# Kernel tuning notes

Hardware: AMD Instinct MI355X
Metric: run time of the kernel (lower is better)

The kernel has to match this reference:

```python
import jax, jax.numpy as jnp
import numpy as np
import math

B, N, D, H = 2, 2048, 512, 8
DK = D // H
MIN_WL, MAX_WL, BASE, EPS = 3.7, 20.0, 20.0, 0.02


def setup_inputs() -> dict:
    key = jax.random.key(0)
    ks = jax.random.split(key, 8)
    q = jax.random.normal(ks[0], (B, N, D), dtype=jnp.float32)
    k = jax.random.normal(ks[1], (B, N, D), dtype=jnp.float32)
    v = jax.random.normal(ks[2], (B, N, D), dtype=jnp.float32)
    coords = jax.random.normal(ks[3], (B, N, 3), dtype=jnp.float32)
    key_padding_mask = jnp.zeros((B, N), dtype=bool)
    q_proj = jax.random.normal(ks[4], (H, D, DK), dtype=jnp.float32)
    k_proj = jax.random.normal(ks[5], (H, D, DK), dtype=jnp.float32)
    v_proj = jax.random.normal(ks[6], (H, D, DK), dtype=jnp.float32)
    out_w = jax.random.normal(ks[7], (D, D), dtype=jnp.float32) / math.sqrt(D)
    out_b = jnp.zeros((D,), dtype=jnp.float32)
    return {"q": q, "k": k, "v": v, "coords": coords,
            "key_padding_mask": key_padding_mask,
            "q_proj": q_proj, "k_proj": k_proj, "v_proj": v_proj,
            "out_w": out_w, "out_b": out_b}


def reference(q, k, v, coords, key_padding_mask, q_proj, k_proj, v_proj, out_w, out_b):
    b, n, d = q.shape
    h, _, dk = q_proj.shape
    # per-head projections: [b,h,n,dk]
    qh = jnp.einsum('bnd,hdk->bhnk', q, q_proj)
    kh = jnp.einsum('bnd,hdk->bhnk', k, k_proj)
    vh = jnp.einsum('bnd,hdk->bhnk', v, v_proj)
    attn = jnp.einsum('bhik,bhjk->bhij', qh, kh) / math.sqrt(dk)  # [b,h,n,n]
    # pairwise distances [b,1,n,n]
    diff = coords[:, :, None, :] - coords[:, None, :, :]
    dists = jnp.sqrt(jnp.sum(diff * diff, axis=-1))[:, None, :, :]
    # per-head spreads via logspace(0, 1-eps, h, base=BASE)
    logsp = BASE ** jnp.linspace(0.0, 1.0 - EPS, h, dtype=jnp.float32)
    spreads = MIN_WL + (logsp - 1.0) / (BASE - 1.0) * (MAX_WL - MIN_WL)
    spreads = spreads[None, :, None, None]  # [1,h,1,1]
    # clamp small dists up to spread, large dists down to 3*spread (masked anyway)
    d1 = jnp.where(dists < spreads, spreads, dists)            # [b,h,n,n]
    dist_mask = d1 > 3.0 * spreads
    d2 = jnp.where(dist_mask, 3.0 * spreads, d1)
    # RBF scaling, inverted where attn < 0
    rbf = jnp.exp(-(d2 * d2) / (2.0 * spreads * spreads))
    rbf = jnp.where(attn < 0, 1.0 / rbf, rbf)
    attn = attn * rbf
    # padding + distance mask, softmax
    mask = key_padding_mask[:, None, None, :] | dist_mask
    attn = jnp.where(mask, -jnp.inf, attn)
    attn = jax.nn.softmax(attn, axis=-1)
    out = jnp.einsum('bhij,bhjk->bhik', attn, vh)  # [b,h,n,dk]
    out = jnp.transpose(out, (0, 2, 1, 3)).reshape(b, n, d)
    return out @ out_w.T + out_b
```

## Files before the change

### kernel.cpp

```cpp
#include <hip/hip_runtime.h>
#include <hip/hip_bf16.h>
#include <cmath>

typedef __attribute__((ext_vector_type(8))) short bf16x8;
typedef __attribute__((ext_vector_type(4))) float f32x4;
typedef __attribute__((ext_vector_type(4))) short short4v;

#define MFMA16(a,b,c) __builtin_amdgcn_mfma_f32_16x16x32_bf16((a),(b),(c),0,0,0)
#define EXP2F(x) __builtin_amdgcn_exp2f(x)
#define GLOAD_LDS16(g, l) __builtin_amdgcn_global_load_lds( \
    (const __attribute__((address_space(1))) unsigned int*)(g), \
    (__attribute__((address_space(3))) unsigned int*)(l), 16, 0, 0)

__device__ __forceinline__ short f2bf(float x){
  unsigned u = __float_as_uint(x);
  u += 0x7fffu + ((u >> 16) & 1u);
  return (short)(u >> 16);
}
__device__ __forceinline__ float bf2f(short h){
  return __uint_as_float(((unsigned)(unsigned short)h) << 16);
}
__device__ __forceinline__ int swz(int row, int c){ return (row << 3) | (c ^ (row & 7)); }

__global__ void split3(const float* __restrict__ q, const float* __restrict__ k,
                       const float* __restrict__ v,
                       short* __restrict__ q_hi, short* __restrict__ q_lo,
                       short* __restrict__ k_hi, short* __restrict__ k_lo,
                       short* __restrict__ v_hi){
  int y = blockIdx.y;
  int i4 = (blockIdx.x * 256 + threadIdx.x) * 4;
  if(y == 0){
    float4 x = *(const float4*)(q + i4);
    short4v hi, lo;
    float xs[4] = {x.x, x.y, x.z, x.w};
    #pragma unroll
    for(int r=0;r<4;r++){ short h = f2bf(xs[r]); hi[r]=h; lo[r]=f2bf(xs[r]-bf2f(h)); }
    *(short4v*)(q_hi + i4) = hi; *(short4v*)(q_lo + i4) = lo;
  } else if(y == 1){
    float4 x = *(const float4*)(k + i4);
    short4v hi, lo;
    float xs[4] = {x.x, x.y, x.z, x.w};
    #pragma unroll
    for(int r=0;r<4;r++){ short h = f2bf(xs[r]); hi[r]=h; lo[r]=f2bf(xs[r]-bf2f(h)); }
    *(short4v*)(k_hi + i4) = hi; *(short4v*)(k_lo + i4) = lo;
  } else {
    float4 x = *(const float4*)(v + i4);
    short4v hi;
    float xs[4] = {x.x, x.y, x.z, x.w};
    #pragma unroll
    for(int r=0;r<4;r++) hi[r] = f2bf(xs[r]);
    *(short4v*)(v_hi + i4) = hi;
  }
}

__global__ void split_proj4(const float* __restrict__ qp, const float* __restrict__ kp,
                            const float* __restrict__ vp, const float* __restrict__ ow,
                            short* __restrict__ BqHi, short* __restrict__ BqLo,
                            short* __restrict__ BkHi, short* __restrict__ BkLo,
                            short* __restrict__ BvHi,
                            short* __restrict__ WHi,  short* __restrict__ WLo){
  int y = blockIdx.y;
  int i = blockIdx.x * 256 + threadIdx.x;
  int n = i >> 9, d = i & 511;
  int h = n >> 6, c = n & 63;
  long si = (long)((h << 15) | (d << 6) | c);
  if(y == 0){
    float x = qp[si]; short hh = f2bf(x);
    BqHi[i] = hh; BqLo[i] = f2bf(x - bf2f(hh));
  } else if(y == 1){
    float x = kp[si]; short hh = f2bf(x);
    BkHi[i] = hh; BkLo[i] = f2bf(x - bf2f(hh));
  } else if(y == 2){
    BvHi[i] = f2bf(vp[si]);
  } else {
    float x = ow[i]; short hh = f2bf(x);
    WHi[i] = hh; WLo[i] = f2bf(x - bf2f(hh));
  }
}

__global__ __launch_bounds__(256) void gemm_qkv(
    const short* __restrict__ q_hi, const short* __restrict__ q_lo,
    const short* __restrict__ k_hi, const short* __restrict__ k_lo,
    const short* __restrict__ v_hi,
    const short* __restrict__ BqHi, const short* __restrict__ BqLo,
    const short* __restrict__ BkHi, const short* __restrict__ BkLo,
    const short* __restrict__ BvHi,
    short* __restrict__ qhHi, short* __restrict__ qhLo,
    short* __restrict__ khHi, short* __restrict__ khLo,
    short* __restrict__ vt)
{
  constexpr int K = 512;
  __shared__ __attribute__((aligned(16))) short sAhi[128*64];
  __shared__ __attribute__((aligned(16))) short sBhi[64*64];
  __shared__ __attribute__((aligned(16))) short sAlo[128*64];
  __shared__ __attribute__((aligned(16))) short sBlo[64*64];
  const int tid = threadIdx.x;
  const int z = blockIdx.z;
  const bool three = (z < 2);
  const short* Ahi = z==0 ? q_hi : z==1 ? k_hi : v_hi;
  const short* Alo = z==0 ? q_lo : k_lo;
  const short* Bhi = z==0 ? BqHi : z==1 ? BkHi : BvHi;
  const short* Blo = z==0 ? BqLo : BkLo;
  const float scale = z==0 ? 0.125f*1.44269504f : 1.f;
  const int m0 = blockIdx.x * 128, n0 = blockIdx.y * 64;
  const int w = tid >> 6, lane = tid & 63;
  const int wm = (w >> 1) * 64, wn = (w & 1) * 32;
  const int lr = lane & 15, lg = lane >> 4;

  f32x4 acc[4][2];
  for(int i=0;i<4;i++) for(int j=0;j<2;j++) acc[i][j] = f32x4{0.f,0.f,0.f,0.f};

  for(int kt = 0; kt < K; kt += 64){
    __syncthreads();
    for(int u = tid; u < 1024; u += 256){
      int row = u >> 3, c = u & 7;
      long ga = (long)(m0 + row) * K + kt + (c ^ (row & 7))*8;
      GLOAD_LDS16(Ahi + ga, sAhi + u*8);
      if(three) GLOAD_LDS16(Alo + ga, sAlo + u*8);
    }
    for(int u = tid; u < 512; u += 256){
      int row = u >> 3, c = u & 7;
      long ga = (long)(n0 + row) * K + kt + (c ^ (row & 7))*8;
      GLOAD_LDS16(Bhi + ga, sBhi + u*8);
      if(three) GLOAD_LDS16(Blo + ga, sBlo + u*8);
    }
    __syncthreads();
    #pragma unroll
    for(int ks = 0; ks < 2; ks++){
      bf16x8 ah[4], al[4], bh[2], bl[2];
      #pragma unroll
      for(int i=0;i<4;i++){
        int row = wm + i*16 + lr, c = ks*4 + lg;
        ah[i] = *(const bf16x8*)(sAhi + swz(row,c)*8);
        if(three) al[i] = *(const bf16x8*)(sAlo + swz(row,c)*8);
      }
      #pragma unroll
      for(int j=0;j<2;j++){
        int row = wn + j*16 + lr, c = ks*4 + lg;
        bh[j] = *(const bf16x8*)(sBhi + swz(row,c)*8);
        if(three) bl[j] = *(const bf16x8*)(sBlo + swz(row,c)*8);
      }
      #pragma unroll
      for(int i=0;i<4;i++)
        #pragma unroll
        for(int j=0;j<2;j++){
          acc[i][j] = MFMA16(ah[i], bh[j], acc[i][j]);
          if(three){
            acc[i][j] = MFMA16(ah[i], bl[j], acc[i][j]);
            acc[i][j] = MFMA16(al[i], bh[j], acc[i][j]);
          }
        }
    }
  }
  #pragma unroll
  for(int i=0;i<4;i++){
    #pragma unroll
    for(int j=0;j<2;j++){
      int row = m0 + wm + i*16 + lg*4;
      int col = n0 + wn + j*16 + lr;
      if(z == 2){
        int bb = row >> 11;
        int hh = col >> 6, cc = col & 63;
        short4v pk;
        #pragma unroll
        for(int r=0;r<4;r++) pk[r] = f2bf(acc[i][j][r]);
        long idx = ((long)((bb*8 + hh)*64 + cc) << 11) + (row & 2047);
        *(short4v*)(vt + idx) = pk;
      } else {
        short* O0 = z==0 ? qhHi : khHi;
        short* O1 = z==0 ? qhLo : khLo;
        #pragma unroll
        for(int r=0;r<4;r++){
          float v = acc[i][j][r] * scale;
          long idx = (long)(row + r) * 512 + col;
          short hh = f2bf(v);
          O0[idx] = hh;
          O1[idx] = f2bf(v - bf2f(hh));
        }
      }
    }
  }
}

template<int NPROD, int EPI>
__global__ __launch_bounds__(256) void gemm_k(
    const short* __restrict__ Ahi, const short* __restrict__ Alo,
    const short* __restrict__ Bhi, const short* __restrict__ Blo,
    short* __restrict__ O0, short* __restrict__ O1,
    float* __restrict__ Of, const float* __restrict__ bias, float scale)
{
  constexpr int K = 512;
  __shared__ __attribute__((aligned(16))) short sAhi[128*64];
  __shared__ __attribute__((aligned(16))) short sBhi[64*64];
  __shared__ __attribute__((aligned(16))) short sAlo[NPROD==3 ? 128*64 : 8];
  __shared__ __attribute__((aligned(16))) short sBlo[NPROD==3 ? 64*64 : 8];
  const int tid = threadIdx.x;
  const int m0 = blockIdx.x * 128, n0 = blockIdx.y * 64;
  const int w = tid >> 6, lane = tid & 63;
  const int wm = (w >> 1) * 64, wn = (w & 1) * 32;
  const int lr = lane & 15, lg = lane >> 4;

  f32x4 acc[4][2];
  for(int i=0;i<4;i++) for(int j=0;j<2;j++) acc[i][j] = f32x4{0.f,0.f,0.f,0.f};

  for(int kt = 0; kt < K; kt += 64){
    __syncthreads();
    for(int u = tid; u < 1024; u += 256){
      int row = u >> 3, c = u & 7;
      long ga = (long)(m0 + row) * K + kt + (c ^ (row & 7))*8;
      GLOAD_LDS16(Ahi + ga, sAhi + u*8);
      if(NPROD == 3) GLOAD_LDS16(Alo + ga, sAlo + u*8);
    }
    for(int u = tid; u < 512; u += 256){
      int row = u >> 3, c = u & 7;
      long ga = (long)(n0 + row) * K + kt + (c ^ (row & 7))*8;
      GLOAD_LDS16(Bhi + ga, sBhi + u*8);
      if(NPROD == 3) GLOAD_LDS16(Blo + ga, sBlo + u*8);
    }
    __syncthreads();
    #pragma unroll
    for(int ks = 0; ks < 2; ks++){
      bf16x8 ah[4], al[4], bh[2], bl[2];
      #pragma unroll
      for(int i=0;i<4;i++){
        int row = wm + i*16 + lr, c = ks*4 + lg;
        ah[i] = *(const bf16x8*)(sAhi + swz(row,c)*8);
        if(NPROD==3) al[i] = *(const bf16x8*)(sAlo + swz(row,c)*8);
      }
      #pragma unroll
      for(int j=0;j<2;j++){
        int row = wn + j*16 + lr, c = ks*4 + lg;
        bh[j] = *(const bf16x8*)(sBhi + swz(row,c)*8);
        if(NPROD==3) bl[j] = *(const bf16x8*)(sBlo + swz(row,c)*8);
      }
      #pragma unroll
      for(int i=0;i<4;i++)
        #pragma unroll
        for(int j=0;j<2;j++){
          acc[i][j] = MFMA16(ah[i], bh[j], acc[i][j]);
          if(NPROD==3){
            acc[i][j] = MFMA16(ah[i], bl[j], acc[i][j]);
            acc[i][j] = MFMA16(al[i], bh[j], acc[i][j]);
          }
        }
    }
  }
  #pragma unroll
  for(int i=0;i<4;i++){
    #pragma unroll
    for(int j=0;j<2;j++){
      int row = m0 + wm + i*16 + lg*4;
      int col = n0 + wn + j*16 + lr;
      if(EPI == 1){
        int bb = row >> 11;
        int hh = col >> 6, cc = col & 63;
        short4v pk;
        #pragma unroll
        for(int r=0;r<4;r++) pk[r] = f2bf(acc[i][j][r] * scale);
        long idx = ((long)((bb*8 + hh)*64 + cc) << 11) + (row & 2047);
        *(short4v*)(O0 + idx) = pk;
      } else {
        #pragma unroll
        for(int r=0;r<4;r++){
          float v = acc[i][j][r] * scale;
          long idx = (long)(row + r) * 512 + col;
          if(EPI == 0){
            short hh = f2bf(v);
            O0[idx] = hh;
            O1[idx] = f2bf(v - bf2f(hh));
          } else {
            Of[idx] = v + bias[col];
          }
        }
      }
    }
  }
}

struct SpreadArgs { float sig2[8]; float nine[8]; float inv2l[8]; };

__global__ __launch_bounds__(256) void attn_k(
    const short* __restrict__ qhHi, const short* __restrict__ qhLo,
    const short* __restrict__ khHi, const short* __restrict__ khLo,
    const short* __restrict__ vt,
    const float* __restrict__ coords,
    const unsigned char* __restrict__ kpm,
    short* __restrict__ Xhi, short* __restrict__ Xlo,
    SpreadArgs sa)
{
  __shared__ __attribute__((aligned(16))) short sKhi[64*64];
  __shared__ __attribute__((aligned(16))) short sKlo[64*64];
  __shared__ __attribute__((aligned(16))) short sV[64*64];
  __shared__ __attribute__((aligned(16))) short sCjPk[64*8];
  __shared__ float sNj[64];
  __shared__ __attribute__((aligned(16))) short sP[4][16][72];

  const int tid = threadIdx.x, w = tid >> 6, lane = tid & 63;
  const int lr = lane & 15, lg = lane >> 4;
  const int L = blockIdx.x;
  const int xcd = L & 7, ix = L >> 3;
  const int pair = xcd*2 + (ix >> 5);
  const int b = pair >> 3, h = pair & 7, i0 = (ix & 31) * 64;
  const float sig2 = sa.sig2[h], nine = sa.nine[h], inv2l = sa.inv2l[h];
  bf16x8 ones8;
  #pragma unroll
  for(int i=0;i<8;i++) ones8[i] = (short)0x3F80;

  long qrow = (long)(b*2048 + i0 + w*16 + lr) * 512 + h*64;
  bf16x8 qhi[2], qlo[2];
  #pragma unroll
  for(int ks=0; ks<2; ks++){
    qhi[ks] = *(const bf16x8*)(qhHi + qrow + ks*32 + lg*8);
    qlo[ks] = *(const bf16x8*)(qhLo + qrow + ks*32 + lg*8);
  }
  bf16x8 ciA;
  #pragma unroll
  for(int i=0;i<8;i++) ciA[i] = 0;
  {
    long cb = (long)(b*2048 + i0 + w*16 + lr)*3;
    #pragma unroll
    for(int e=0;e<3;e++){
      float c = coords[cb + e];
      short chi = f2bf(c);
      short clo = f2bf(c - bf2f(chi));
      ciA[e] = f2bf(-2.f * bf2f(lg < 2 ? chi : clo));
    }
  }
  float ni[4];
  {
    int r0 = b*2048 + i0 + w*16 + lg*4;
    #pragma unroll
    for(int r=0;r<4;r++){
      float cx = coords[(long)(r0+r)*3 + 0];
      float cy = coords[(long)(r0+r)*3 + 1];
      float cz = coords[(long)(r0+r)*3 + 2];
      ni[r] = cx*cx + cy*cy + cz*cz;
    }
  }
  f32x4 oacc[4];
  for(int c=0;c<4;c++) oacc[c] = f32x4{0.f,0.f,0.f,0.f};
  float m[4], l[4];
  for(int r=0;r<4;r++){ m[r] = -1e30f; l[r] = 0.f; }

  for(int jt=0; jt<32; jt++){
    int j0 = jt*64;
    for(int u=tid; u<512; u+=256){
      int row = u>>3, cc = u&7;
      int cs = cc ^ (row & 7);
      long gk = (long)(b*2048 + j0 + row)*512 + h*64 + cs*8;
      GLOAD_LDS16(khHi + gk, sKhi + u*8);
      GLOAD_LDS16(khLo + gk, sKlo + u*8);
      long gv = ((long)((b*8+h)*64 + row) << 11) + j0 + cs*8;
      GLOAD_LDS16(vt + gv, sV + u*8);
    }
    if(tid < 64){
      long cb = (long)(b*2048 + j0 + tid)*3;
      float cx = coords[cb], cy = coords[cb+1], cz = coords[cb+2];
      short hx = f2bf(cx), hy = f2bf(cy), hz = f2bf(cz);
      bf16x8 pk;
      pk[0] = hx; pk[1] = hy; pk[2] = hz; pk[3] = 0;
      pk[4] = f2bf(cx - bf2f(hx));
      pk[5] = f2bf(cy - bf2f(hy));
      pk[6] = f2bf(cz - bf2f(hz));
      pk[7] = 0;
      *(bf16x8*)(sCjPk + tid*8) = pk;
      sNj[tid] = cx*cx + cy*cy + cz*cz + (kpm[b*2048 + j0 + tid] ? 1e37f : 0.f);
    }
    __syncthreads();

    f32x4 s[4];
    #pragma unroll
    for(int jf=0;jf<4;jf++){
      f32x4 t = f32x4{0.f,0.f,0.f,0.f};
      #pragma unroll
      for(int ks=0;ks<2;ks++){
        int row = jf*16 + lr, c = ks*4 + lg;
        bf16x8 bh = *(const bf16x8*)(sKhi + swz(row,c)*8);
        bf16x8 bl = *(const bf16x8*)(sKlo + swz(row,c)*8);
        t = MFMA16(qhi[ks], bh, t);
        t = MFMA16(qhi[ks], bl, t);
        t = MFMA16(qlo[ks], bh, t);
      }
      s[jf] = t;
    }
    f32x4 d2t[4];
    #pragma unroll
    for(int jf=0;jf<4;jf++){
      bf16x8 cjB;
      #pragma unroll
      for(int i=0;i<8;i++) cjB[i] = 0;
      {
        short4v c4 = *(const short4v*)(sCjPk + (jf*16 + lr)*8 + (lg & 1)*4);
        cjB[0] = c4[0]; cjB[1] = c4[1]; cjB[2] = c4[2];
      }
      float njv = sNj[jf*16 + lr];
      f32x4 cin;
      #pragma unroll
      for(int r=0;r<4;r++) cin[r] = ni[r] + njv;
      d2t[jf] = MFMA16(ciA, cjB, cin);
    }
    #pragma unroll
    for(int jf=0;jf<4;jf++){
      #pragma unroll
      for(int r=0;r<4;r++){
        float d2 = d2t[jf][r];
        float tt = fminf(fmaxf(d2, sig2), nine);
        float arg2 = tt * inv2l;
        float sv = s[jf][r];
        sv *= EXP2F(sv < 0.f ? arg2 : -arg2);
        if(d2 > nine) sv = -1e30f;
        s[jf][r] = sv;
      }
    }
    float pm[4];
    #pragma unroll
    for(int r=0;r<4;r++)
      pm[r] = fmaxf(fmaxf(s[0][r], s[1][r]), fmaxf(s[2][r], s[3][r]));
    #pragma unroll
    for(int d=1; d<16; d<<=1){
      #pragma unroll
      for(int r=0;r<4;r++) pm[r] = fmaxf(pm[r], __shfl_xor(pm[r], d));
    }
    float fr[4];
    #pragma unroll
    for(int r=0;r<4;r++){
      float mn = fmaxf(m[r], pm[r]);
      fr[r] = EXP2F(m[r] - mn);
      m[r] = mn;
      l[r] *= fr[r];
    }
    #pragma unroll
    for(int jf=0;jf<4;jf++)
      #pragma unroll
      for(int r=0;r<4;r++)
        s[jf][r] = EXP2F(s[jf][r] - m[r]);
    #pragma unroll
    for(int c=0;c<4;c++)
      #pragma unroll
      for(int r=0;r<4;r++) oacc[c][r] *= fr[r];
    #pragma unroll
    for(int jf=0;jf<4;jf++)
      #pragma unroll
      for(int r=0;r<4;r++)
        sP[w][lg*4 + r][jf*16 + lr] = f2bf(s[jf][r]);
    f32x4 psacc = f32x4{0.f,0.f,0.f,0.f};
    #pragma unroll
    for(int js=0;js<2;js++){
      union { bf16x8 v8; short4v h4[2]; } pa;
      pa.h4[0] = *(const short4v*)(&sP[w][lr][js*32 + lg*8]);
      pa.h4[1] = *(const short4v*)(&sP[w][lr][js*32 + lg*8 + 4]);
      #pragma unroll
      for(int cf=0; cf<4; cf++){
        int vrow = cf*16 + lr, vc = js*4 + lg;
        bf16x8 vb = *(const bf16x8*)(sV + swz(vrow,vc)*8);
        oacc[cf] = MFMA16(pa.v8, vb, oacc[cf]);
      }
      psacc = MFMA16(pa.v8, ones8, psacc);
    }
    #pragma unroll
    for(int r=0;r<4;r++) l[r] += psacc[r];
    __syncthreads();
  }
  #pragma unroll
  for(int cf=0; cf<4; cf++){
    #pragma unroll
    for(int r=0;r<4;r++){
      float v = oacc[cf][r] / l[r];
      long idx = (long)(b*2048 + i0 + w*16 + lg*4 + r)*512 + h*64 + cf*16 + lr;
      short hh = f2bf(v);
      Xhi[idx] = hh;
      Xlo[idx] = f2bf(v - bf2f(hh));
    }
  }
}

extern "C" void kernel_launch(void* const* d_in, const int* in_sizes, int n_in,
                              void* d_out, int out_size, void* d_ws, size_t ws_size,
                              hipStream_t stream){
  const float* q  = (const float*)d_in[0];
  const float* k  = (const float*)d_in[1];
  const float* v  = (const float*)d_in[2];
  const float* coords = (const float*)d_in[3];
  const unsigned char* kpm = (const unsigned char*)d_in[4];
  const float* qp = (const float*)d_in[5];
  const float* kp = (const float*)d_in[6];
  const float* vp = (const float*)d_in[7];
  const float* ow = (const float*)d_in[8];
  const float* ob = (const float*)d_in[9];
  float* out = (float*)d_out;

  char* ws = (char*)d_ws;
  const size_t S = (size_t)4096*512*2;
  const size_t P = (size_t)512*512*2;
  if(ws_size < 12*S + 7*P) return;
  short* q_hi = (short*)(ws + 0*S);
  short* q_lo = (short*)(ws + 1*S);
  short* k_hi = (short*)(ws + 2*S);
  short* k_lo = (short*)(ws + 3*S);
  short* v_hi = (short*)(ws + 4*S);
  short* qhHi = (short*)(ws + 5*S);
  short* qhLo = (short*)(ws + 6*S);
  short* khHi = (short*)(ws + 7*S);
  short* khLo = (short*)(ws + 8*S);
  short* vt   = (short*)(ws + 9*S);
  short* Xhi  = (short*)(ws + 10*S);
  short* Xlo  = (short*)(ws + 11*S);
  char* ws2 = ws + 12*S;
  short* BqHi = (short*)(ws2 + 0*P);
  short* BqLo = (short*)(ws2 + 1*P);
  short* BkHi = (short*)(ws2 + 2*P);
  short* BkLo = (short*)(ws2 + 3*P);
  short* BvHi = (short*)(ws2 + 4*P);
  short* WHi  = (short*)(ws2 + 5*P);
  short* WLo  = (short*)(ws2 + 6*P);

  SpreadArgs sa;
  for(int hh=0; hh<8; hh++){
    double t  = (1.0 - 0.02) * (double)hh / 7.0;
    double lg = pow(20.0, t);
    double sp = 3.7 + (lg - 1.0) / 19.0 * (20.0 - 3.7);
    float spf = (float)sp;
    sa.sig2[hh] = spf*spf;
    sa.nine[hh] = 9.f*spf*spf;
    sa.inv2l[hh] = 1.44269504f/(2.f*spf*spf);
  }

  const int NQ = 4096*512;
  split3<<<dim3(NQ/1024, 3), dim3(256), 0, stream>>>(q, k, v, q_hi, q_lo, k_hi, k_lo, v_hi);
  split_proj4<<<dim3(1024, 4), dim3(256), 0, stream>>>(qp, kp, vp, ow,
      BqHi, BqLo, BkHi, BkLo, BvHi, WHi, WLo);

  gemm_qkv<<<dim3(32, 8, 3), dim3(256), 0, stream>>>(
      q_hi, q_lo, k_hi, k_lo, v_hi,
      BqHi, BqLo, BkHi, BkLo, BvHi,
      qhHi, qhLo, khHi, khLo, vt);

  attn_k<<<dim3(512), dim3(256), 0, stream>>>(qhHi, qhLo, khHi, khLo, vt,
        coords, kpm, Xhi, Xlo, sa);

  gemm_k<3,2><<<dim3(32, 8), dim3(256), 0, stream>>>(Xhi, Xlo, WHi, WLo,
        nullptr, nullptr, out, ob, 1.f);
}
```

Measured before the change: 144.3 us.

## Transpose score MFMAs so each lane owns one query row in softmax

The QK^T and distance MFMAs now take swapped operands, so the score tile comes out transposed and each lane holds all values for a single query row. Row max and row sum then need only two cross-lane shuffles instead of a four-step butterfly over four rows. The ones-vector MFMA that computed row sums is removed, and P is written to LDS with packed bf16 conversion stores. This adds shuffles to redistribute the rescale factors and the final normaliser back to the output accumulator layout.

Measured after the change: 136.7 us. 5.2% less time.

```diff
diff --git a/kernel.cpp b/kernel.cpp
--- a/kernel.cpp
+++ b/kernel.cpp
@@ -5,6 +5,7 @@
 typedef __attribute__((ext_vector_type(8))) short bf16x8;
 typedef __attribute__((ext_vector_type(4))) float f32x4;
 typedef __attribute__((ext_vector_type(4))) short short4v;
+typedef __attribute__((ext_vector_type(2))) unsigned int uint2v;
 
 #define MFMA16(a,b,c) __builtin_amdgcn_mfma_f32_16x16x32_bf16((a),(b),(c),0,0,0)
 #define EXP2F(x) __builtin_amdgcn_exp2f(x)
@@ -19,6 +20,11 @@
 }
 __device__ __forceinline__ float bf2f(short h){
   return __uint_as_float(((unsigned)(unsigned short)h) << 16);
+}
+__device__ __forceinline__ unsigned cvtpk_bf16(float a, float b){
+  unsigned r;
+  asm("v_cvt_pk_bf16_f32 %0, %1, %2" : "=v"(r) : "v"(a), "v"(b));
+  return r;
 }
 __device__ __forceinline__ int swz(int row, int c){ return (row << 3) | (c ^ (row & 7)); }
 
@@ -292,7 +298,7 @@
   __shared__ __attribute__((aligned(16))) short sKlo[64*64];
   __shared__ __attribute__((aligned(16))) short sV[64*64];
   __shared__ __attribute__((aligned(16))) short sCjPk[64*8];
-  __shared__ float sNj[64];
+  __shared__ __attribute__((aligned(16))) float sNj[64];
   __shared__ __attribute__((aligned(16))) short sP[4][16][72];
 
   const int tid = threadIdx.x, w = tid >> 6, lane = tid & 63;
@@ -302,9 +308,6 @@
   const int pair = xcd*2 + (ix >> 5);
   const int b = pair >> 3, h = pair & 7, i0 = (ix & 31) * 64;
   const float sig2 = sa.sig2[h], nine = sa.nine[h], inv2l = sa.inv2l[h];
-  bf16x8 ones8;
-  #pragma unroll
-  for(int i=0;i<8;i++) ones8[i] = (short)0x3F80;
 
   long qrow = (long)(b*2048 + i0 + w*16 + lr) * 512 + h*64;
   bf16x8 qhi[2], qlo[2];
@@ -313,34 +316,25 @@
     qhi[ks] = *(const bf16x8*)(qhHi + qrow + ks*32 + lg*8);
     qlo[ks] = *(const bf16x8*)(qhLo + qrow + ks*32 + lg*8);
   }
-  bf16x8 ciA;
+  bf16x8 ciB;
   #pragma unroll
-  for(int i=0;i<8;i++) ciA[i] = 0;
+  for(int i=0;i<8;i++) ciB[i] = 0;
+  float ni;
   {
     long cb = (long)(b*2048 + i0 + w*16 + lr)*3;
+    float c0 = coords[cb], c1 = coords[cb+1], c2 = coords[cb+2];
+    float cs[3] = {c0, c1, c2};
     #pragma unroll
     for(int e=0;e<3;e++){
-      float c = coords[cb + e];
-      short chi = f2bf(c);
-      short clo = f2bf(c - bf2f(chi));
-      ciA[e] = f2bf(-2.f * bf2f(lg < 2 ? chi : clo));
-    }
-  }
-  float ni[4];
-  {
-    int r0 = b*2048 + i0 + w*16 + lg*4;
-    #pragma unroll
-    for(int r=0;r<4;r++){
-      float cx = coords[(long)(r0+r)*3 + 0];
-      float cy = coords[(long)(r0+r)*3 + 1];
-      float cz = coords[(long)(r0+r)*3 + 2];
-      ni[r] = cx*cx + cy*cy + cz*cz;
-    }
+      short chi = f2bf(cs[e]);
+      short clo = f2bf(cs[e] - bf2f(chi));
+      ciB[e] = ((lg & 1) == 0) ? chi : clo;
+    }
+    ni = c0*c0 + c1*c1 + c2*c2;
   }
   f32x4 oacc[4];
   for(int c=0;c<4;c++) oacc[c] = f32x4{0.f,0.f,0.f,0.f};
-  float m[4], l[4];
-  for(int r=0;r<4;r++){ m[r] = -1e30f; l[r] = 0.f; }
+  float m = -1e30f, l = 0.f;
 
   for(int jt=0; jt<32; jt++){
     int j0 = jt*64;
@@ -356,12 +350,13 @@
     if(tid < 64){
       long cb = (long)(b*2048 + j0 + tid)*3;
       float cx = coords[cb], cy = coords[cb+1], cz = coords[cb+2];
-      short hx = f2bf(cx), hy = f2bf(cy), hz = f2bf(cz);
+      float mx = -2.f*cx, my = -2.f*cy, mz = -2.f*cz;
+      short hx = f2bf(mx), hy = f2bf(my), hz = f2bf(mz);
       bf16x8 pk;
       pk[0] = hx; pk[1] = hy; pk[2] = hz; pk[3] = 0;
-      pk[4] = f2bf(cx - bf2f(hx));
-      pk[5] = f2bf(cy - bf2f(hy));
-      pk[6] = f2bf(cz - bf2f(hz));
+      pk[4] = f2bf(mx - bf2f(hx));
+      pk[5] = f2bf(my - bf2f(hy));
+      pk[6] = f2bf(mz - bf2f(hz));
       pk[7] = 0;
       *(bf16x8*)(sCjPk + tid*8) = pk;
       sNj[tid] = cx*cx + cy*cy + cz*cz + (kpm[b*2048 + j0 + tid] ? 1e37f : 0.f);
@@ -377,33 +372,29 @@
         int row = jf*16 + lr, c = ks*4 + lg;
         bf16x8 bh = *(const bf16x8*)(sKhi + swz(row,c)*8);
         bf16x8 bl = *(const bf16x8*)(sKlo + swz(row,c)*8);
-        t = MFMA16(qhi[ks], bh, t);
-        t = MFMA16(qhi[ks], bl, t);
-        t = MFMA16(qlo[ks], bh, t);
+        t = MFMA16(bh, qhi[ks], t);
+        t = MFMA16(bl, qhi[ks], t);
+        t = MFMA16(bh, qlo[ks], t);
       }
       s[jf] = t;
     }
-    f32x4 d2t[4];
     #pragma unroll
     for(int jf=0;jf<4;jf++){
-      bf16x8 cjB;
-      #pragma unroll
-      for(int i=0;i<8;i++) cjB[i] = 0;
+      bf16x8 cjA;
+      #pragma unroll
+      for(int i=0;i<8;i++) cjA[i] = 0;
       {
-        short4v c4 = *(const short4v*)(sCjPk + (jf*16 + lr)*8 + (lg & 1)*4);
-        cjB[0] = c4[0]; cjB[1] = c4[1]; cjB[2] = c4[2];
-      }
-      float njv = sNj[jf*16 + lr];
+        short4v c4 = *(const short4v*)(sCjPk + (jf*16 + lr)*8 + (lg >> 1)*4);
+        cjA[0] = c4[0]; cjA[1] = c4[1]; cjA[2] = c4[2];
+      }
+      f32x4 nj4 = *(const f32x4*)(sNj + jf*16 + lg*4);
       f32x4 cin;
       #pragma unroll
-      for(int r=0;r<4;r++) cin[r] = ni[r] + njv;
-      d2t[jf] = MFMA16(ciA, cjB, cin);
-    }
-    #pragma unroll
-    for(int jf=0;jf<4;jf++){
+      for(int r=0;r<4;r++) cin[r] = ni + nj4[r];
+      f32x4 d2t = MFMA16(cjA, ciB, cin);
       #pragma unroll
       for(int r=0;r<4;r++){
-        float d2 = d2t[jf][r];
+        float d2 = d2t[r];
         float tt = fminf(fmaxf(d2, sig2), nine);
         float arg2 = tt * inv2l;
         float sv = s[jf][r];
@@ -412,60 +403,62 @@
         s[jf][r] = sv;
       }
     }
-    float pm[4];
-    #pragma unroll
-    for(int r=0;r<4;r++)
-      pm[r] = fmaxf(fmaxf(s[0][r], s[1][r]), fmaxf(s[2][r], s[3][r]));
-    #pragma unroll
-    for(int d=1; d<16; d<<=1){
-      #pragma unroll
-      for(int r=0;r<4;r++) pm[r] = fmaxf(pm[r], __shfl_xor(pm[r], d));
-    }
-    float fr[4];
-    #pragma unroll
-    for(int r=0;r<4;r++){
-      float mn = fmaxf(m[r], pm[r]);
-      fr[r] = EXP2F(m[r] - mn);
-      m[r] = mn;
-      l[r] *= fr[r];
-    }
+    float pm = s[0][0];
     #pragma unroll
     for(int jf=0;jf<4;jf++)
       #pragma unroll
-      for(int r=0;r<4;r++)
-        s[jf][r] = EXP2F(s[jf][r] - m[r]);
+      for(int r=0;r<4;r++) pm = fmaxf(pm, s[jf][r]);
+    pm = fmaxf(pm, __shfl_xor(pm, 16));
+    pm = fmaxf(pm, __shfl_xor(pm, 32));
+    float mn = fmaxf(m, pm);
+    float fr = EXP2F(m - mn);
+    m = mn;
+    float ps = 0.f;
+    #pragma unroll
+    for(int jf=0;jf<4;jf++)
+      #pragma unroll
+      for(int r=0;r<4;r++){
+        float p = EXP2F(s[jf][r] - m);
+        s[jf][r] = p;
+        ps += p;
+      }
+    ps += __shfl_xor(ps, 16);
+    ps += __shfl_xor(ps, 32);
+    l = l*fr + ps;
+    float frq[4];
+    #pragma unroll
+    for(int r=0;r<4;r++) frq[r] = __shfl(fr, lg*4 + r);
     #pragma unroll
     for(int c=0;c<4;c++)
       #pragma unroll
-      for(int r=0;r<4;r++) oacc[c][r] *= fr[r];
-    #pragma unroll
-    for(int jf=0;jf<4;jf++)
-      #pragma unroll
-      for(int r=0;r<4;r++)
-        sP[w][lg*4 + r][jf*16 + lr] = f2bf(s[jf][r]);
-    f32x4 psacc = f32x4{0.f,0.f,0.f,0.f};
+      for(int r=0;r<4;r++) oacc[c][r] *= frq[r];
+    #pragma unroll
+    for(int jf=0;jf<4;jf++){
+      uint2v wds;
+      wds.x = cvtpk_bf16(s[jf][0], s[jf][1]);
+      wds.y = cvtpk_bf16(s[jf][2], s[jf][3]);
+      *(uint2v*)(&sP[w][lr][jf*16 + lg*4]) = wds;
+    }
     #pragma unroll
     for(int js=0;js<2;js++){
-      union { bf16x8 v8; short4v h4[2]; } pa;
-      pa.h4[0] = *(const short4v*)(&sP[w][lr][js*32 + lg*8]);
-      pa.h4[1] = *(const short4v*)(&sP[w][lr][js*32 + lg*8 + 4]);
+      bf16x8 pa = *(const bf16x8*)(&sP[w][lr][js*32 + lg*8]);
       #pragma unroll
       for(int cf=0; cf<4; cf++){
         int vrow = cf*16 + lr, vc = js*4 + lg;
         bf16x8 vb = *(const bf16x8*)(sV + swz(vrow,vc)*8);
-        oacc[cf] = MFMA16(pa.v8, vb, oacc[cf]);
-      }
-      psacc = MFMA16(pa.v8, ones8, psacc);
-    }
-    #pragma unroll
-    for(int r=0;r<4;r++) l[r] += psacc[r];
+        oacc[cf] = MFMA16(pa, vb, oacc[cf]);
+      }
+    }
     __syncthreads();
   }
+  float lq[4];
+  #pragma unroll
+  for(int r=0;r<4;r++) lq[r] = __shfl(l, lg*4 + r);
   #pragma unroll
   for(int cf=0; cf<4; cf++){
     #pragma unroll
     for(int r=0;r<4;r++){
-      float v = oacc[cf][r] / l[r];
+      float v = oacc[cf][r] / lq[r];
       long idx = (long)(b*2048 + i0 + w*16 + lg*4 + r)*512 + h*64 + cf*16 + lr;
       short hh = f2bf(v);
       Xhi[idx] = hh;
```
